# Kernel optimization log

Hardware: AMD Instinct MI355X
Metric: run time of the kernel (lower is better)

The kernel has to match this reference:

```python
import jax, jax.numpy as jnp
import numpy as np

B, H, S, D = 4, 16, 2048, 64


def setup_inputs() -> dict:
    key = jax.random.key(0)
    kq, kk, kv = jax.random.split(key, 3)
    q = jax.random.normal(kq, (B, H, S, D), dtype=jnp.float32)
    k = jax.random.normal(kk, (B, H, S, D), dtype=jnp.float32)
    v = jax.random.normal(kv, (B, H, S, D), dtype=jnp.float32)
    # causal mask: 1 = keep, 0 = masked (matches masked_fill(mask == 0, -10000))
    mask = jnp.tril(jnp.ones((S, S), dtype=jnp.int32))[None, None, :, :]
    return {"q": q, "k": k, "v": v, "mask": mask}


def reference(q, k, v, mask):
    head_dim = q.shape[3]
    # [b,h,s,t] attention logits
    attn = jnp.einsum("bhsd,bhtd->bhst", q, k) / jnp.sqrt(jnp.float32(head_dim))
    attn = jnp.where(mask == 0, jnp.float32(-10000.0), attn)
    score = jax.nn.softmax(attn, axis=-1)
    # dropout is identity at inference (eval mode)
    return jnp.einsum("bhst,bhtd->bhsd", score, v)
```

## Files before the change

### kernel.cpp

```cpp
#include <hip/hip_runtime.h>
#include <hip/hip_bf16.h>

typedef __bf16 bf16_t;
typedef bf16_t bf16x8 __attribute__((ext_vector_type(8)));
typedef float  f32x4  __attribute__((ext_vector_type(4)));
typedef float  f32x16 __attribute__((ext_vector_type(16)));
typedef int    i32x4  __attribute__((ext_vector_type(4)));

#define DH 64

__device__ __forceinline__ unsigned pkbf(float a, float b) {
    union { bf16_t h[2]; unsigned u; } z;
    z.h[0] = (bf16_t)a; z.h[1] = (bf16_t)b;
    return z.u;
}

#define EXP2F(x) exp2f(x)


__global__ __launch_bounds__(256, 2)
void sdpa_fwd(const float* __restrict__ Qg, const float* __restrict__ Kg,
              const float* __restrict__ Vg, float* __restrict__ Og)
{
    __shared__ char lds[2 * 16384];

    const int n  = blockIdx.x;
    const int o  = ((n & 7) << 6) | (n >> 3);
    const int bh = o >> 3;
    const int pr = o & 7;

    const int t   = threadIdx.x;
    const int w   = t >> 6;
    const int l31 = t & 31;
    const int hi  = (t >> 5) & 1;
    const int swk = (l31 & 7) << 4;

    const size_t hoff = (size_t)bh * 2048 * DH;
    const float* Qh = Qg + hoff;
    const float* Kh = Kg + hoff;
    const float* Vh = Vg + hoff;
    float*       Oh = Og + hoff;

    const int srow = (t >> 3) * 2;
    const int sdc  = t & 7;

    const int p0  = 15 - pr;
    const int nk0 = 2 * p0 + 2;
    const int NT  = 34;

    f32x4 rk[4], rv[4];

    auto loadKV = [&](int key0) {
        const float* kp = Kh + (size_t)(key0 + srow) * DH + sdc * 8;
        rk[0] = *(const f32x4*)kp;        rk[1] = *(const f32x4*)(kp + 4);
        rk[2] = *(const f32x4*)(kp + DH); rk[3] = *(const f32x4*)(kp + DH + 4);
        const float* vp = Vh + (size_t)(key0 + srow) * DH + sdc * 8;
        rv[0] = *(const f32x4*)vp;        rv[1] = *(const f32x4*)(vp + 4);
        rv[2] = *(const f32x4*)(vp + DH); rv[3] = *(const f32x4*)(vp + DH + 4);
    };
    auto stageTo = [&](char* kb_, char* vb_) {
#pragma unroll
        for (int r2 = 0; r2 < 2; ++r2) {
            const int key = srow + r2;
            union { unsigned u[4]; bf16x8 v; } f;
            f.u[0] = pkbf(rk[r2*2][0],   rk[r2*2][1]);
            f.u[1] = pkbf(rk[r2*2][2],   rk[r2*2][3]);
            f.u[2] = pkbf(rk[r2*2+1][0], rk[r2*2+1][1]);
            f.u[3] = pkbf(rk[r2*2+1][2], rk[r2*2+1][3]);
            *(bf16x8*)(kb_ + ((key * 128 + sdc * 16) ^ ((key & 7) << 4))) = f.v;
        }
#pragma unroll
        for (int jj = 0; jj < 8; ++jj) {
            const int d  = sdc * 8 + jj;
            const float x0 = (jj < 4) ? rv[0][jj & 3] : rv[1][jj & 3];
            const float x1 = (jj < 4) ? rv[2][jj & 3] : rv[3][jj & 3];
            *(unsigned*)(vb_ + ((d * 128 + srow * 2) ^ (((jj ^ sdc) & 7) << 4)))
                = pkbf(x0, x1);
        }
    };
    auto keybase = [&](int g) { return ((g < nk0) ? g : g - nk0) * 64; };

    const float QSCALE = 0.125f * 1.44269504088896f;

    bf16x8 ones;
#pragma unroll
    for (int j = 0; j < 8; ++j) ones[j] = (bf16_t)1.0f;

    loadKV(0);
    stageTo(lds, lds + 8192);
    loadKV(keybase(1));
    __syncthreads();

    int gt = 0;
    const int stripes[2] = { p0, pr };
    for (int s = 0; s < 2; ++s) {
        const int p    = stripes[s];
        const int h    = 2 * p + 2;
        const int qsb  = p * 128 + w * 32;
        const int qrow = qsb + l31;
        const int ktd  = qsb >> 6;

        bf16x8 qf[4];
#pragma unroll
        for (int sd = 0; sd < 4; ++sd) {
            const float* qp = Qh + (size_t)qrow * DH + sd * 16 + hi * 8;
            f32x4 a = *(const f32x4*)qp;
            f32x4 b = *(const f32x4*)(qp + 4);
            union { unsigned u[4]; bf16x8 v; } f;
            f.u[0] = pkbf(a[0]*QSCALE, a[1]*QSCALE);
            f.u[1] = pkbf(a[2]*QSCALE, a[3]*QSCALE);
            f.u[2] = pkbf(b[0]*QSCALE, b[1]*QSCALE);
            f.u[3] = pkbf(b[2]*QSCALE, b[3]*QSCALE);
            qf[sd] = f.v;
        }

        f32x16 acc0 = {}, acc1 = {};
        f32x16 accS = {};

        for (int i = 0; i < h; ++i, ++gt) {
            char* cb_ = lds + (gt & 1) * 16384;
            char* sb_ = lds + ((gt + 1) & 1) * 16384;

            if (gt + 1 < NT) stageTo(sb_, sb_ + 8192);
            if (gt + 2 < NT) loadKV(keybase(gt + 2));

            if (i <= ktd) {
                char* kb_ = cb_;
                char* vb_ = cb_ + 8192;

                f32x16 tf0 = {}, tf1 = {};
                __builtin_amdgcn_s_setprio(1);
#pragma unroll
                for (int sd = 0; sd < 4; ++sd) {
                    const int inner = sd * 32 + hi * 16;
                    const bf16x8 k0 = *(const bf16x8*)(kb_ + ((l31 * 128 + inner) ^ swk));
                    const bf16x8 k1 = *(const bf16x8*)(kb_ + (((32 + l31) * 128 + inner) ^ swk));
                    tf0 = __builtin_amdgcn_mfma_f32_32x32x16_bf16(k0, qf[sd], tf0, 0, 0, 0);
                    tf1 = __builtin_amdgcn_mfma_f32_32x32x16_bf16(k1, qf[sd], tf1, 0, 0, 0);
                }
                __builtin_amdgcn_s_setprio(0);

                if (i == ktd) {
#pragma unroll
                    for (int rr = 0; rr < 16; ++rr) {
                        const int krow = i * 64 + (rr & 3) + 8 * (rr >> 2) + 4 * hi;
                        if (krow > qrow)      tf0[rr] = -20000.0f;
                        if (krow + 32 > qrow) tf1[rr] = -20000.0f;
                    }
                }

#pragma unroll
                for (int rr = 0; rr < 16; ++rr) tf0[rr] = EXP2F(tf0[rr]);
#pragma unroll
                for (int rr = 0; rr < 16; ++rr) tf1[rr] = EXP2F(tf1[rr]);

                unsigned P0[2][4], P1[2][4];
#pragma unroll
                for (int rg = 0; rg < 4; ++rg) {
                    P0[0][rg] = pkbf(tf0[rg * 4 + 0], tf0[rg * 4 + 1]);
                    P1[0][rg] = pkbf(tf0[rg * 4 + 2], tf0[rg * 4 + 3]);
                    P0[1][rg] = pkbf(tf1[rg * 4 + 0], tf1[rg * 4 + 1]);
                    P1[1][rg] = pkbf(tf1[rg * 4 + 2], tf1[rg * 4 + 3]);
                }

                __builtin_amdgcn_s_setprio(1);
#pragma unroll
                for (int sidx = 0; sidx < 4; ++sidx) {
                    const int kb  = sidx >> 1;
                    const int rgl = (sidx & 1) * 2, rgh = rgl + 1;
                    int w0, w1, w2, w3;
#if defined(__has_builtin) && __has_builtin(__builtin_amdgcn_permlane32_swap)
                    auto r0 = __builtin_amdgcn_permlane32_swap((int)P0[kb][rgl], (int)P0[kb][rgh], false, false);
                    auto r1 = __builtin_amdgcn_permlane32_swap((int)P1[kb][rgl], (int)P1[kb][rgh], false, false);
                    w0 = r0[0]; w2 = r0[1]; w1 = r1[0]; w3 = r1[1];
#else
                    const int sa0 = __shfl_xor((int)P0[kb][rgl], 32);
                    const int sb0 = __shfl_xor((int)P0[kb][rgh], 32);
                    const int sa1 = __shfl_xor((int)P1[kb][rgl], 32);
                    const int sb1 = __shfl_xor((int)P1[kb][rgh], 32);
                    w0 = hi ? sb0 : (int)P0[kb][rgl];
                    w2 = hi ? (int)P0[kb][rgh] : sa0;
                    w1 = hi ? sb1 : (int)P1[kb][rgl];
                    w3 = hi ? (int)P1[kb][rgh] : sa1;
#endif
                    union { i32x4 ii; bf16x8 v; } pz;
                    pz.ii = (i32x4){ w0, w1, w2, w3 };

                    const int inner = sidx * 32 + hi * 16;
                    const int d0 = l31;
                    const int d1 = 32 + l31;
                    const int sz0 = (((d0 & 7) ^ (d0 >> 3)) & 7) << 4;
                    const int sz1 = (((d1 & 7) ^ (d1 >> 3)) & 7) << 4;
                    const bf16x8 v0 = *(const bf16x8*)(vb_ + ((d0 * 128 + inner) ^ sz0));
                    const bf16x8 v1 = *(const bf16x8*)(vb_ + ((d1 * 128 + inner) ^ sz1));
                    acc0 = __builtin_amdgcn_mfma_f32_32x32x16_bf16(v0, pz.v, acc0, 0, 0, 0);
                    acc1 = __builtin_amdgcn_mfma_f32_32x32x16_bf16(v1, pz.v, acc1, 0, 0, 0);
                    accS = __builtin_amdgcn_mfma_f32_32x32x16_bf16(ones, pz.v, accS, 0, 0, 0);
                }
                __builtin_amdgcn_s_setprio(0);
            }
            __syncthreads();
        }

        const float inv = 1.0f / accS[0];
        float* op = Oh + (size_t)qrow * DH;
#pragma unroll
        for (int rq = 0; rq < 4; ++rq) {
            f32x4 o0, o1;
#pragma unroll
            for (int j = 0; j < 4; ++j) {
                o0[j] = acc0[rq * 4 + j] * inv;
                o1[j] = acc1[rq * 4 + j] * inv;
            }
            *(f32x4*)(op + 8 * rq + 4 * hi)      = o0;
            *(f32x4*)(op + 32 + 8 * rq + 4 * hi) = o1;
        }
    }
}

extern "C" void kernel_launch(void* const* d_in, const int* in_sizes, int n_in,
                              void* d_out, int out_size, void* d_ws, size_t ws_size,
                              hipStream_t stream) {
    (void)in_sizes; (void)n_in; (void)d_ws; (void)ws_size; (void)out_size;
    const float* q = (const float*)d_in[0];
    const float* k = (const float*)d_in[1];
    const float* v = (const float*)d_in[2];
    float* out = (float*)d_out;
    hipLaunchKernelGGL(sdpa_fwd, dim3(512), dim3(256), 0, stream, q, k, v, out);
}
```

Baseline: 84.50 us.

## Software-pipeline PV matmul one tile behind QK with triple-buffered LDS

Moves to three LDS buffers so the P·V MFMAs for the previous key tile run in the same iteration as the QK MFMAs and exp for the current tile, letting matrix and transcendental work overlap. It also drops the ones-vector MFMA used for the softmax denominator and instead sums the exponentials in registers with one cross-half shuffle. The cost is 48KB of LDS per block, which may limit occupancy at launch bound 2, plus extra registers to hold the pending P fragments.

```diff
diff --git a/kernel.cpp b/kernel.cpp
--- a/kernel.cpp
+++ b/kernel.cpp
@@ -22,7 +22,7 @@
 void sdpa_fwd(const float* __restrict__ Qg, const float* __restrict__ Kg,
               const float* __restrict__ Vg, float* __restrict__ Og)
 {
-    __shared__ char lds[2 * 16384];
+    __shared__ char lds[3 * 16384];
 
     const int n  = blockIdx.x;
     const int o  = ((n & 7) << 6) | (n >> 3);
@@ -82,16 +82,38 @@
 
     const float QSCALE = 0.125f * 1.44269504088896f;
 
-    bf16x8 ones;
-#pragma unroll
-    for (int j = 0; j < 8; ++j) ones[j] = (bf16_t)1.0f;
-
     loadKV(0);
     stageTo(lds, lds + 8192);
     loadKV(keybase(1));
     __syncthreads();
 
-    int gt = 0;
+    int gt  = 0;
+    int cur = 0;
+    unsigned Pp[16];
+#pragma unroll
+    for (int z = 0; z < 16; ++z) Pp[z] = 0;
+    f32x16 acc0 = {}, acc1 = {};
+
+    auto doPV = [&](char* vb_) {
+        __builtin_amdgcn_s_setprio(1);
+#pragma unroll
+        for (int sidx = 0; sidx < 4; ++sidx) {
+            union { i32x4 ii; bf16x8 v; } pz;
+            pz.ii = (i32x4){ (int)Pp[sidx*4+0], (int)Pp[sidx*4+1],
+                             (int)Pp[sidx*4+2], (int)Pp[sidx*4+3] };
+            const int inner = sidx * 32 + hi * 16;
+            const int d0 = l31;
+            const int d1 = 32 + l31;
+            const int sz0 = (((d0 & 7) ^ (d0 >> 3)) & 7) << 4;
+            const int sz1 = (((d1 & 7) ^ (d1 >> 3)) & 7) << 4;
+            const bf16x8 v0 = *(const bf16x8*)(vb_ + ((d0 * 128 + inner) ^ sz0));
+            const bf16x8 v1 = *(const bf16x8*)(vb_ + ((d1 * 128 + inner) ^ sz1));
+            acc0 = __builtin_amdgcn_mfma_f32_32x32x16_bf16(v0, pz.v, acc0, 0, 0, 0);
+            acc1 = __builtin_amdgcn_mfma_f32_32x32x16_bf16(v1, pz.v, acc1, 0, 0, 0);
+        }
+        __builtin_amdgcn_s_setprio(0);
+    };
+
     const int stripes[2] = { p0, pr };
     for (int s = 0; s < 2; ++s) {
         const int p    = stripes[s];
@@ -114,29 +136,32 @@
             qf[sd] = f.v;
         }
 
-        f32x16 acc0 = {}, acc1 = {};
-        f32x16 accS = {};
+        acc0 = (f32x16){}; acc1 = (f32x16){};
+        float l_run = 0.0f;
 
         for (int i = 0; i < h; ++i, ++gt) {
-            char* cb_ = lds + (gt & 1) * 16384;
-            char* sb_ = lds + ((gt + 1) & 1) * 16384;
+            const int nxt = (cur + 1 == 3) ? 0 : cur + 1;
+            const int prv = (cur == 0) ? 2 : cur - 1;
+            char* cb_ = lds + cur * 16384;
+            char* sb_ = lds + nxt * 16384;
+            char* pb_ = lds + prv * 16384;
 
             if (gt + 1 < NT) stageTo(sb_, sb_ + 8192);
             if (gt + 2 < NT) loadKV(keybase(gt + 2));
 
+            if (i > 0 && (i - 1) <= ktd) doPV(pb_ + 8192);
+
             if (i <= ktd) {
-                char* kb_ = cb_;
-                char* vb_ = cb_ + 8192;
-
-                f32x16 tf0 = {}, tf1 = {};
+                f32x16 tf = {};
+                f32x16 tg = {};
                 __builtin_amdgcn_s_setprio(1);
 #pragma unroll
                 for (int sd = 0; sd < 4; ++sd) {
                     const int inner = sd * 32 + hi * 16;
-                    const bf16x8 k0 = *(const bf16x8*)(kb_ + ((l31 * 128 + inner) ^ swk));
-                    const bf16x8 k1 = *(const bf16x8*)(kb_ + (((32 + l31) * 128 + inner) ^ swk));
-                    tf0 = __builtin_amdgcn_mfma_f32_32x32x16_bf16(k0, qf[sd], tf0, 0, 0, 0);
-                    tf1 = __builtin_amdgcn_mfma_f32_32x32x16_bf16(k1, qf[sd], tf1, 0, 0, 0);
+                    const bf16x8 k0 = *(const bf16x8*)(cb_ + ((l31 * 128 + inner) ^ swk));
+                    const bf16x8 k1 = *(const bf16x8*)(cb_ + (((32 + l31) * 128 + inner) ^ swk));
+                    tf = __builtin_amdgcn_mfma_f32_32x32x16_bf16(k0, qf[sd], tf, 0, 0, 0);
+                    tg = __builtin_amdgcn_mfma_f32_32x32x16_bf16(k1, qf[sd], tg, 0, 0, 0);
                 }
                 __builtin_amdgcn_s_setprio(0);
 
@@ -144,26 +169,27 @@
 #pragma unroll
                     for (int rr = 0; rr < 16; ++rr) {
                         const int krow = i * 64 + (rr & 3) + 8 * (rr >> 2) + 4 * hi;
-                        if (krow > qrow)      tf0[rr] = -20000.0f;
-                        if (krow + 32 > qrow) tf1[rr] = -20000.0f;
+                        if (krow > qrow)      tf[rr] = -20000.0f;
+                        if (krow + 32 > qrow) tg[rr] = -20000.0f;
                     }
                 }
 
-#pragma unroll
-                for (int rr = 0; rr < 16; ++rr) tf0[rr] = EXP2F(tf0[rr]);
-#pragma unroll
-                for (int rr = 0; rr < 16; ++rr) tf1[rr] = EXP2F(tf1[rr]);
+                float sum = 0.0f;
+#pragma unroll
+                for (int rr = 0; rr < 16; ++rr) { tf[rr] = EXP2F(tf[rr]); sum += tf[rr]; }
+#pragma unroll
+                for (int rr = 0; rr < 16; ++rr) { tg[rr] = EXP2F(tg[rr]); sum += tg[rr]; }
+                sum += __shfl_xor(sum, 32);
+                l_run += sum;
 
                 unsigned P0[2][4], P1[2][4];
 #pragma unroll
                 for (int rg = 0; rg < 4; ++rg) {
-                    P0[0][rg] = pkbf(tf0[rg * 4 + 0], tf0[rg * 4 + 1]);
-                    P1[0][rg] = pkbf(tf0[rg * 4 + 2], tf0[rg * 4 + 3]);
-                    P0[1][rg] = pkbf(tf1[rg * 4 + 0], tf1[rg * 4 + 1]);
-                    P1[1][rg] = pkbf(tf1[rg * 4 + 2], tf1[rg * 4 + 3]);
-                }
-
-                __builtin_amdgcn_s_setprio(1);
+                    P0[0][rg] = pkbf(tf[rg * 4 + 0], tf[rg * 4 + 1]);
+                    P1[0][rg] = pkbf(tf[rg * 4 + 2], tf[rg * 4 + 3]);
+                    P0[1][rg] = pkbf(tg[rg * 4 + 0], tg[rg * 4 + 1]);
+                    P1[1][rg] = pkbf(tg[rg * 4 + 2], tg[rg * 4 + 3]);
+                }
 #pragma unroll
                 for (int sidx = 0; sidx < 4; ++sidx) {
                     const int kb  = sidx >> 1;
@@ -183,26 +209,22 @@
                     w1 = hi ? sb1 : (int)P1[kb][rgl];
                     w3 = hi ? (int)P1[kb][rgh] : sa1;
 #endif
-                    union { i32x4 ii; bf16x8 v; } pz;
-                    pz.ii = (i32x4){ w0, w1, w2, w3 };
-
-                    const int inner = sidx * 32 + hi * 16;
-                    const int d0 = l31;
-                    const int d1 = 32 + l31;
-                    const int sz0 = (((d0 & 7) ^ (d0 >> 3)) & 7) << 4;
-                    const int sz1 = (((d1 & 7) ^ (d1 >> 3)) & 7) << 4;
-                    const bf16x8 v0 = *(const bf16x8*)(vb_ + ((d0 * 128 + inner) ^ sz0));
-                    const bf16x8 v1 = *(const bf16x8*)(vb_ + ((d1 * 128 + inner) ^ sz1));
-                    acc0 = __builtin_amdgcn_mfma_f32_32x32x16_bf16(v0, pz.v, acc0, 0, 0, 0);
-                    acc1 = __builtin_amdgcn_mfma_f32_32x32x16_bf16(v1, pz.v, acc1, 0, 0, 0);
-                    accS = __builtin_amdgcn_mfma_f32_32x32x16_bf16(ones, pz.v, accS, 0, 0, 0);
-                }
-                __builtin_amdgcn_s_setprio(0);
+                    Pp[sidx*4+0] = (unsigned)w0;
+                    Pp[sidx*4+1] = (unsigned)w1;
+                    Pp[sidx*4+2] = (unsigned)w2;
+                    Pp[sidx*4+3] = (unsigned)w3;
+                }
             }
             __syncthreads();
-        }
-
-        const float inv = 1.0f / accS[0];
+            cur = nxt;
+        }
+
+        if (ktd == h - 1) {
+            const int prv = (cur == 0) ? 2 : cur - 1;
+            doPV(lds + prv * 16384 + 8192);
+        }
+
+        const float inv = 1.0f / l_run;
         float* op = Oh + (size_t)qrow * DH;
 #pragma unroll
         for (int rq = 0; rq < 4; ++rq) {
```

Result: slower. 88.51 us (+4.7%).
